# Optimization experiments

Measured on AMD Instinct MI355X. Metric: run time of the kernel, lower is better.

## Reference

```python
import jax, jax.numpy as jnp
import numpy as np

B, H, W, C, K = 16, 64, 64, 512, 32
MAX_ITERS = 20  # module hardcodes max_iters=20; tol check replaced by fixed trip count (converged state is a fixed point)
EPS = 1e-12


def _l2_normalize(v):
    return v / jnp.maximum(jnp.linalg.norm(v, axis=-1, keepdims=True), EPS)


def setup_inputs() -> dict:
    key = jax.random.key(0)
    x = jax.random.normal(key, (B, H, W, C), dtype=jnp.float32)
    rng = np.random.default_rng(0)
    N = H * W
    # per-batch distinct initial centroid indices (mirrors numpy Generator.choice without replacement)
    init_idx = jnp.asarray(np.stack([rng.choice(N, K, replace=False) for _ in range(B)]), dtype=jnp.int32)
    return {"x": x, "init_idx": init_idx}


def reference(x, init_idx):
    Bq, Hq, Wq, Cq = x.shape
    N = Hq * Wq
    xf = _l2_normalize(x.reshape(Bq, N, Cq))  # [B,N,C], unit-norm points
    # gather initial centroids xf[b, init_idx[b,k]] -> [B,K,C]
    c0 = jnp.take_along_axis(xf, init_idx[:, :, None].astype(jnp.int32), axis=1)

    def step(c, _):
        sim = jnp.einsum('bnc,bkc->bnk', xf, c)          # cosine similarity
        assign = jnp.argmax(sim, axis=-1)                # [B,N] hard assignment
        onehot = jax.nn.one_hot(assign, c.shape[1], dtype=xf.dtype)  # [B,N,K]
        sums = jnp.einsum('bnk,bnc->bkc', onehot, xf)    # scatter-sum via dense one-hot matmul
        counts = jnp.sum(onehot, axis=1)[:, :, None]     # [B,K,1]
        mean = sums / jnp.maximum(counts, 1.0)
        new_c = jnp.where(counts > 0, mean, c)           # keep old centroid for empty clusters
        return _l2_normalize(new_c), None                # spherical k-means: renormalize centroids

    c, _ = jax.lax.scan(step, c0, None, length=MAX_ITERS)
    return c  # [B,K,C]
```

## Files before the change

### kernel.cpp

```cpp
#include <hip/hip_runtime.h>
#include <hip/hip_cooperative_groups.h>
#include <cstddef>

namespace cg = cooperative_groups;

constexpr int Bb = 16;
constexpr int Cc = 512;
constexpr int Kk = 32;
constexpr int Nn = 64 * 64;
constexpr int ITERS = 20;

constexpr int TPB  = 1024;
constexpr int PPB  = 256;
constexpr int SUBS = Nn / PPB;
constexpr int GRID = Bb * SUBS;

constexpr float SCALE_F   = 1099511627776.0f;
constexpr float INVSCALE  = 1.0f / 1099511627776.0f;

__global__ __launch_bounds__(TPB, 4)
void kmeans_fused(const float* __restrict__ x, const int* __restrict__ idx,
                  float* __restrict__ out,
                  float* __restrict__ invn, float* __restrict__ cent,
                  long long* __restrict__ psums, int* __restrict__ pcounts,
                  int* __restrict__ assign, int* __restrict__ flags)
{
    cg::grid_group gg = cg::this_grid();
    const int t   = threadIdx.x;
    const int bid = blockIdx.x;
    const int b   = bid >> 4;
    const int sub = bid & (SUBS - 1);
    const int base = sub * PPB;

    __shared__ float s_buf[Kk * Cc];
    int*       s_asg  = (int*)(s_buf + 1024);
    int*       s_old  = (int*)(s_buf + 1280);
    float*     s_inv  = s_buf + 1536;
    long long* s_sums = (long long*)(s_buf + 2048);
    float*     s_red  = s_buf;

    {
        const int gtid = bid * TPB + t;
        const int p    = gtid >> 2;
        const int qd   = gtid & 3;
        const float* xr = x + (size_t)p * Cc + qd * 128;
        float ss = 0.f;
        #pragma unroll
        for (int c0 = 0; c0 < 128; c0 += 4) {
            float4 v = *(const float4*)(xr + c0);
            ss = fmaf(v.x, v.x, fmaf(v.y, v.y, fmaf(v.z, v.z, fmaf(v.w, v.w, ss))));
        }
        ss += __shfl_xor(ss, 1);
        ss += __shfl_xor(ss, 2);
        if (qd == 0) invn[p] = 1.0f / fmaxf(sqrtf(ss), 1e-12f);
        for (int e = gtid; e < Bb * Kk * Cc; e += GRID * TPB) psums[e] = 0;
        if (gtid < Bb * Kk) pcounts[gtid] = 0;
        if (gtid < ITERS)   flags[gtid] = 0;
        for (int e = gtid; e < Bb * Nn; e += GRID * TPB) assign[e] = -1;
    }
    gg.sync();

    {
        const int gtid = bid * TPB + t;
        for (int e = gtid; e < Bb * Kk * Cc; e += GRID * TPB) {
            const int c  = e & (Cc - 1);
            const int bk = e >> 9;
            const int k  = bk & (Kk - 1);
            const int bb = bk >> 5;
            const int pid = idx[bb * Kk + k];
            cent[e] = x[((size_t)bb * Nn + pid) * Cc + c] * invn[bb * Nn + pid];
        }
    }
    gg.sync();

    const float* xb = x + (size_t)b * Nn * Cc;

    for (int it = 0; it < ITERS; ++it) {
        if (it > 0) {
            int ch = __hip_atomic_load(&flags[it - 1], __ATOMIC_RELAXED,
                                       __HIP_MEMORY_SCOPE_AGENT);
            if (ch == 0) break;
        }

        {
            const float* cbp = cent + (size_t)b * Kk * Cc;
            #pragma unroll
            for (int e = 4 * t; e < Kk * Cc; e += 4 * TPB)
                *(float4*)(s_buf + e) = *(const float4*)(cbp + e);
        }
        __syncthreads();

        const int p  = t >> 2;
        const int qo = (t & 3) * 4;
        const int n  = base + p;
        const float* xr = xb + (size_t)n * Cc;

        float sim[Kk];
        #pragma unroll
        for (int k = 0; k < Kk; ++k) sim[k] = 0.f;

        float4 xv = *(const float4*)(xr + qo);
        for (int c0 = 0; c0 < Cc; c0 += 16) {
            const int cn = (c0 + 16 < Cc) ? (c0 + 16) : 0;
            const float4 xn = *(const float4*)(xr + cn + qo);
            const float* cl = s_buf + c0 + qo;
            #pragma unroll
            for (int k = 0; k < Kk; ++k) {
                const float4 cf = *(const float4*)(cl + k * Cc);
                sim[k] = fmaf(xv.x, cf.x,
                         fmaf(xv.y, cf.y,
                         fmaf(xv.z, cf.z,
                         fmaf(xv.w, cf.w, sim[k]))));
            }
            xv = xn;
        }
        #pragma unroll
        for (int k = 0; k < Kk; ++k) {
            sim[k] += __shfl_xor(sim[k], 1);
            sim[k] += __shfl_xor(sim[k], 2);
        }
        float best = sim[0]; int bki = 0;
        #pragma unroll
        for (int k = 1; k < Kk; ++k)
            if (sim[k] > best) { best = sim[k]; bki = k; }

        __syncthreads();

        if ((t & 3) == 0) {
            const int prev = assign[b * Nn + n];
            if (bki != prev) {
                atomicOr(&flags[it], 1);
                atomicAdd(&pcounts[b * Kk + bki], 1);
                if (prev >= 0) atomicAdd(&pcounts[b * Kk + prev], -1);
                assign[b * Nn + n] = bki;
            }
            s_asg[p] = bki;
            s_old[p] = prev;
            s_inv[p] = invn[b * Nn + n];
        }
        __syncthreads();

        const int col_l = t & 127;
        const int h     = (t >> 7) & 7;
        for (int pass = 0; pass < 4; ++pass) {
            for (int e = t; e < Kk * 128; e += TPB) s_sums[e] = 0;
            __syncthreads();
            const int col = pass * 128 + col_l;
            for (int j = 0; j < 32; ++j) {
                const int p2 = h * 32 + j;
                const int a  = s_asg[p2];
                const int o  = s_old[p2];
                if (a == o) continue;
                const float sc = s_inv[p2];
                const float v  = xb[(size_t)(base + p2) * Cc + col];
                const long long q = (long long)(v * sc * SCALE_F);
                atomicAdd((unsigned long long*)&s_sums[a * 128 + col_l],
                          (unsigned long long)q);
                if (o >= 0)
                    atomicAdd((unsigned long long*)&s_sums[o * 128 + col_l],
                              (unsigned long long)(-q));
            }
            __syncthreads();
            for (int e = t; e < Kk * 128; e += TPB) {
                const long long q = s_sums[e];
                if (q != 0) {
                    const int k = e >> 7;
                    const int c = (e & 127) + pass * 128;
                    atomicAdd((unsigned long long*)&psums[((size_t)b * Kk + k) * Cc + c],
                              (unsigned long long)q);
                }
            }
            __syncthreads();
        }
        gg.sync();

        for (int r = 0; r < 2; ++r) {
            const int ci = 2 * bid + r;
            float* crow = cent + (size_t)ci * Cc;
            float m = 0.f;
            if (t < Cc) {
                const long long q = psums[(size_t)ci * Cc + t];
                const int cnt = pcounts[ci];
                const float s = (float)q * INVSCALE;
                m = (cnt > 0) ? (s / (float)cnt) : crow[t];
            }
            float ss = m * m;
            #pragma unroll
            for (int o = 32; o > 0; o >>= 1) ss += __shfl_down(ss, o, 64);
            if ((t & 63) == 0) s_red[t >> 6] = ss;
            __syncthreads();
            float tot = 0.f;
            #pragma unroll
            for (int w = 0; w < TPB / 64; ++w) tot += s_red[w];
            if (t < Cc) crow[t] = m * (1.0f / fmaxf(sqrtf(tot), 1e-12f));
            __syncthreads();
        }
        gg.sync();
    }

    {
        const int gtid = bid * TPB + t;
        for (int e = gtid; e < Bb * Kk * Cc; e += GRID * TPB)
            out[e] = cent[e];
    }
}

extern "C" void kernel_launch(void* const* d_in, const int* in_sizes, int n_in,
                              void* d_out, int out_size, void* d_ws, size_t ws_size,
                              hipStream_t stream) {
    const float* x  = (const float*)d_in[0];
    const int* idx  = (const int*)d_in[1];
    float* out      = (float*)d_out;

    char* ws = (char*)d_ws;
    size_t off = 0;
    long long* psums = (long long*)(ws + off); off += (size_t)Bb * Kk * Cc * 8;
    float* invn      = (float*)(ws + off);     off += (size_t)Bb * Nn * 4;
    float* cent      = (float*)(ws + off);     off += (size_t)Bb * Kk * Cc * 4;
    int*   pcounts   = (int*)  (ws + off);     off += (size_t)Bb * Kk * 4;
    int*   assign    = (int*)  (ws + off);     off += (size_t)Bb * Nn * 4;
    int*   flags     = (int*)  (ws + off);     off += (size_t)ITERS * 4;

    void* args[] = { (void*)&x, (void*)&idx, (void*)&out, (void*)&invn,
                     (void*)&cent, (void*)&psums, (void*)&pcounts,
                     (void*)&assign, (void*)&flags };
    hipLaunchCooperativeKernel((const void*)kmeans_fused, dim3(GRID), dim3(TPB),
                               args, 0, stream);
}
```

Measured before the change: 3.017 ms.

## Register-tile similarity over 4 points x 8 centroids with swizzled LDS centroids

The similarity loop is restructured so each thread computes a 4-point by 8-centroid tile instead of one point against all 32 centroids. Each centroid float4 read from shared memory is now reused across four points, which cuts LDS traffic per FMA. Centroids are stored with a row-dependent rotation to avoid bank conflicts. The argmax becomes a cross-lane shuffle reduction that breaks ties toward the lower index, and global x reads are now strided across four rows per thread, which may hurt coalescing.

```diff
diff --git a/kernel.cpp b/kernel.cpp
--- a/kernel.cpp
+++ b/kernel.cpp
@@ -83,60 +83,98 @@
         }
 
         {
-            const float* cbp = cent + (size_t)b * Kk * Cc;
-            #pragma unroll
-            for (int e = 4 * t; e < Kk * Cc; e += 4 * TPB)
-                *(float4*)(s_buf + e) = *(const float4*)(cbp + e);
+            const float4* cbp = (const float4*)(cent + (size_t)b * Kk * Cc);
+            float4* sb4 = (float4*)s_buf;
+            #pragma unroll
+            for (int e = t; e < Kk * 128; e += TPB) {
+                const int cl = e >> 7, ch = e & 127;
+                sb4[(cl << 7) | ((ch + 2 * (cl >> 3)) & 127)] = cbp[e];
+            }
         }
         __syncthreads();
 
-        const int p  = t >> 2;
-        const int qo = (t & 3) * 4;
-        const int n  = base + p;
-        const float* xr = xb + (size_t)n * Cc;
-
-        float sim[Kk];
-        #pragma unroll
-        for (int k = 0; k < Kk; ++k) sim[k] = 0.f;
-
-        float4 xv = *(const float4*)(xr + qo);
-        for (int c0 = 0; c0 < Cc; c0 += 16) {
-            const int cn = (c0 + 16 < Cc) ? (c0 + 16) : 0;
-            const float4 xn = *(const float4*)(xr + cn + qo);
-            const float* cl = s_buf + c0 + qo;
-            #pragma unroll
-            for (int k = 0; k < Kk; ++k) {
-                const float4 cf = *(const float4*)(cl + k * Cc);
-                sim[k] = fmaf(xv.x, cf.x,
-                         fmaf(xv.y, cf.y,
-                         fmaf(xv.z, cf.z,
-                         fmaf(xv.w, cf.w, sim[k]))));
-            }
-            xv = xn;
-        }
-        #pragma unroll
-        for (int k = 0; k < Kk; ++k) {
-            sim[k] += __shfl_xor(sim[k], 1);
-            sim[k] += __shfl_xor(sim[k], 2);
-        }
-        float best = sim[0]; int bki = 0;
-        #pragma unroll
-        for (int k = 1; k < Kk; ++k)
-            if (sim[k] > best) { best = sim[k]; bki = k; }
+        const int pg = t >> 4;
+        const int cg = (t >> 2) & 3;
+        const int qd = t & 3;
+        const int p0 = pg << 2;
+        const float* xr0 = xb + (size_t)(base + p0) * Cc;
+        const float4* sb4 = (const float4*)s_buf;
+        const int ro   = qd + 2 * cg;
+        const int cbase = cg << 10;
+
+        float sim[4][8];
+        #pragma unroll
+        for (int i = 0; i < 4; ++i)
+            #pragma unroll
+            for (int l = 0; l < 8; ++l) sim[i][l] = 0.f;
+
+        float4 xf[4];
+        #pragma unroll
+        for (int i = 0; i < 4; ++i)
+            xf[i] = *(const float4*)(xr0 + (size_t)i * Cc + 4 * qd);
+        for (int j = 0; j < 32; ++j) {
+            float4 xn[4];
+            const int chn = (qd + 4 * ((j + 1) & 31)) << 2;
+            #pragma unroll
+            for (int i = 0; i < 4; ++i)
+                xn[i] = *(const float4*)(xr0 + (size_t)i * Cc + chn);
+            const int lc = (ro + 4 * j) & 127;
+            #pragma unroll
+            for (int l = 0; l < 8; ++l) {
+                const float4 cf = sb4[cbase + (l << 7) + lc];
+                #pragma unroll
+                for (int i = 0; i < 4; ++i)
+                    sim[i][l] = fmaf(xf[i].x, cf.x,
+                                fmaf(xf[i].y, cf.y,
+                                fmaf(xf[i].z, cf.z,
+                                fmaf(xf[i].w, cf.w, sim[i][l]))));
+            }
+            #pragma unroll
+            for (int i = 0; i < 4; ++i) xf[i] = xn[i];
+        }
+
+        #pragma unroll
+        for (int i = 0; i < 4; ++i)
+            #pragma unroll
+            for (int l = 0; l < 8; ++l) {
+                sim[i][l] += __shfl_xor(sim[i][l], 1);
+                sim[i][l] += __shfl_xor(sim[i][l], 2);
+            }
+
+        float bv4[4]; int bi4[4];
+        #pragma unroll
+        for (int i = 0; i < 4; ++i) {
+            float bv = sim[i][0]; int bi = cg * 8;
+            #pragma unroll
+            for (int l = 1; l < 8; ++l)
+                if (sim[i][l] > bv) { bv = sim[i][l]; bi = cg * 8 + l; }
+            #pragma unroll
+            for (int m = 4; m <= 8; m <<= 1) {
+                const float ov = __shfl_xor(bv, m);
+                const int   oi = __shfl_xor(bi, m);
+                if (ov > bv || (ov == bv && oi < bi)) { bv = ov; bi = oi; }
+            }
+            bv4[i] = bv; bi4[i] = bi;
+        }
 
         __syncthreads();
 
-        if ((t & 3) == 0) {
-            const int prev = assign[b * Nn + n];
-            if (bki != prev) {
-                atomicOr(&flags[it], 1);
-                atomicAdd(&pcounts[b * Kk + bki], 1);
-                if (prev >= 0) atomicAdd(&pcounts[b * Kk + prev], -1);
-                assign[b * Nn + n] = bki;
-            }
-            s_asg[p] = bki;
-            s_old[p] = prev;
-            s_inv[p] = invn[b * Nn + n];
+        if ((t & 15) == 0) {
+            #pragma unroll
+            for (int i = 0; i < 4; ++i) {
+                const int n   = base + p0 + i;
+                const int bki = bi4[i];
+                const int prev = assign[b * Nn + n];
+                if (bki != prev) {
+                    atomicOr(&flags[it], 1);
+                    atomicAdd(&pcounts[b * Kk + bki], 1);
+                    if (prev >= 0) atomicAdd(&pcounts[b * Kk + prev], -1);
+                    assign[b * Nn + n] = bki;
+                }
+                s_asg[p0 + i] = bki;
+                s_old[p0 + i] = prev;
+                s_inv[p0 + i] = invn[b * Nn + n];
+            }
         }
         __syncthreads();
 
```

Result: no change. 3.027 ms (+0.3%).
